# Performance work log

Hardware: AMD Instinct MI355X
Metric: run time of the kernel (lower is better)

Reference implementation:

```python
import jax, jax.numpy as jnp
from jax import lax
import numpy as np


def _gaussian_kernels(k, sigma):
    # spatial Gaussian kernel per sample; sigma: (B,) -> (B, k, k), normalized
    coords = jnp.arange(k) - k // 2
    grid = (coords[None, :] ** 2 + coords[:, None] ** 2).astype(jnp.float32)
    ker = jnp.exp(-grid[None, :, :] / (2.0 * sigma[:, None, None] ** 2))
    return ker / ker.sum(axis=(1, 2), keepdims=True)


def setup_inputs() -> dict:
    key = jax.random.key(0)
    kx, kp = jax.random.split(key)
    x = jax.random.normal(kx, (8, 64, 384, 384), dtype=jnp.float32)
    params = jax.random.normal(kp, (8, 2), dtype=jnp.float32)
    return {"x": x, "params": params}


def reference(x, params):
    B, C, H, W = x.shape
    # torch: params[:,0].long() truncates toward zero, then sigmoid, then int()
    k_int = jnp.trunc(params[:, 0])
    k_sel = jnp.floor(5.0 + 5.0 * jax.nn.sigmoid(k_int)).astype(jnp.int32)  # (B,) in {5..9}
    sigma = 0.5 + 4.5 * jax.nn.sigmoid(params[:, 1])                        # (B,)

    out = jnp.zeros_like(x)
    # small fixed set of possible kernel sizes (structurally distinct convs)
    for k in range(5, 10):
        ker = _gaussian_kernels(k, sigma)  # (B, k, k)
        pad = k // 2

        def conv_one(xi, ki, pad=pad):
            # depthwise conv with the same (k,k) kernel for every channel:
            # treat channels as batch, single-in single-out kernel.
            y = lax.conv_general_dilated(xi[:, None], ki[None, None],
                                         window_strides=(1, 1),
                                         padding=[(pad, pad), (pad, pad)])
            return y[:, 0]

        y = jax.vmap(conv_one)(x, ker)  # (B, C, H', W'); H'=H+1 when k even
        if k % 2 == 0:
            # F.interpolate bilinear align_corners=False == half-pixel, no antialias
            y = jax.image.resize(y, (B, C, H, W), method='bilinear', antialias=False)
        out = jnp.where((k_sel == k)[:, None, None, None], y, out)
    return out
```

## Files before the change

### kernel.cpp

```cpp
#include <hip/hip_runtime.h>
#include <math.h>

#define B_  8
#define C_  64
#define H_  384
#define W_  384

#define TX   64
#define TY   32
#define HALO 4
#define SW   (TX + 2*HALO)
#define SH   (TY + 2*HALO)
#define SWP  76
#define TXP  68

template<int K>
__device__ __forceinline__ void process_tile(
    float (*sIn)[SWP], float (*sTmp)[TXP],
    float* __restrict__ op, int tx0, int ty0, float sigma, int tid)
{
    constexpr int  PAD  = K / 2;
    constexpr bool EVEN = ((K & 1) == 0);

    float g[K];
    {
        const float inv2s2 = 1.0f / (2.0f * sigma * sigma);
        float S = 0.0f;
        #pragma unroll
        for (int i = 0; i < K; ++i) {
            float d = (float)(i - PAD);
            g[i] = expf(-d * d * inv2s2);
            S += g[i];
        }
        const float invS = 1.0f / S;
        #pragma unroll
        for (int i = 0; i < K; ++i) g[i] *= invS;
    }

    for (int li = tid; li < SH * 8; li += 256) {
        const int r  = li >> 3;
        const int g8 = (li & 7) * 8;
        float V[16];
        #pragma unroll
        for (int i = 0; i < 16; ++i) V[i] = sIn[r][g8 + i];
        #pragma unroll
        for (int j = 0; j < 8; ++j) {
            float a0 = 0.0f;
            #pragma unroll
            for (int t = 0; t < K; ++t) a0 += g[t] * V[j + 4 - PAD + t];
            float val = a0;
            if (EVEN) {
                float a1 = 0.0f;
                #pragma unroll
                for (int t = 0; t < K; ++t) a1 += g[t] * V[j + 5 - PAD + t];
                const float fw = ((float)(tx0 + g8 + j) + 0.5f) * (1.0f / (float)W_);
                val = a0 + fw * (a1 - a0);
            }
            sTmp[r][g8 + j] = val;
        }
    }
    __syncthreads();

    for (int li = tid; li < (TY / 4) * 64; li += 256) {
        const int yg = li >> 6;
        const int xx = li & 63;
        float U[12];
        #pragma unroll
        for (int i = 0; i < 12; ++i) U[i] = sTmp[yg * 4 + i][xx];
        #pragma unroll
        for (int j = 0; j < 4; ++j) {
            float a0 = 0.0f;
            #pragma unroll
            for (int t = 0; t < K; ++t) a0 += g[t] * U[j + 4 - PAD + t];
            float val = a0;
            if (EVEN) {
                float a1 = 0.0f;
                #pragma unroll
                for (int t = 0; t < K; ++t) a1 += g[t] * U[j + 5 - PAD + t];
                const float fh = ((float)(ty0 + yg * 4 + j) + 0.5f) * (1.0f / (float)H_);
                val = a0 + fh * (a1 - a0);
            }
            op[(size_t)(ty0 + yg * 4 + j) * W_ + (tx0 + xx)] = val;
        }
    }
}

__global__ __launch_bounds__(256) void gauss_blur_kernel(
    const float* __restrict__ x, const float* __restrict__ params,
    float* __restrict__ out)
{
    const int b    = blockIdx.z;
    const int c    = blockIdx.y;
    const int tile = blockIdx.x;
    const int ntx  = W_ / TX;
    const int tx0  = (tile % ntx) * TX;
    const int ty0  = (tile / ntx) * TY;

    const float p0 = params[2 * b + 0];
    const float p1 = params[2 * b + 1];
    const float k_int = truncf(p0);
    const float s0 = 1.0f / (1.0f + expf(-k_int));
    int k = (int)floorf(5.0f + 5.0f * s0);
    if (k < 5) k = 5;
    if (k > 9) k = 9;
    const float sigma = 0.5f + 4.5f * (1.0f / (1.0f + expf(-p1)));

    __shared__ float sIn[SH][SWP];
    __shared__ float sTmp[SH][TXP];

    const size_t plane = (size_t)(b * C_ + c) * (size_t)(H_ * W_);
    const float* xp = x + plane;
    float*       op = out + plane;
    const int tid = threadIdx.x;

    for (int li = tid; li < SH * (SW / 4); li += 256) {
        const int r  = li / (SW / 4);
        const int c4 = li - r * (SW / 4);
        const int gr = ty0 - HALO + r;
        const int gc = tx0 - HALO + c4 * 4;
        float4 v = make_float4(0.f, 0.f, 0.f, 0.f);
        if (gr >= 0 && gr < H_ && gc >= 0 && gc < W_)
            v = *reinterpret_cast<const float4*>(xp + (size_t)gr * W_ + gc);
        *reinterpret_cast<float4*>(&sIn[r][c4 * 4]) = v;
    }
    __syncthreads();

    switch (k) {
        case 5:  process_tile<5>(sIn, sTmp, op, tx0, ty0, sigma, tid); break;
        case 6:  process_tile<6>(sIn, sTmp, op, tx0, ty0, sigma, tid); break;
        case 7:  process_tile<7>(sIn, sTmp, op, tx0, ty0, sigma, tid); break;
        case 8:  process_tile<8>(sIn, sTmp, op, tx0, ty0, sigma, tid); break;
        default: process_tile<9>(sIn, sTmp, op, tx0, ty0, sigma, tid); break;
    }
}

extern "C" void kernel_launch(void* const* d_in, const int* in_sizes, int n_in,
                              void* d_out, int out_size, void* d_ws, size_t ws_size,
                              hipStream_t stream) {
    const float* x      = (const float*)d_in[0];
    const float* params = (const float*)d_in[1];
    float* out          = (float*)d_out;

    dim3 grid((W_ / TX) * (H_ / TY), C_, B_);
    dim3 block(256, 1, 1);
    gauss_blur_kernel<<<grid, block, 0, stream>>>(x, params, out);
}
```

Measured before the change: 488.7 us.

## Load input directly into registers, enlarge tiles, and remap blocks across XCDs

Drops the shared-memory input staging pass and its barrier. The horizontal pass now reads float4 rows straight from global memory into registers and writes its results to shared memory as float4. Tiles grow to 128x64 with 512-thread blocks, which cuts halo overhead. The grid is flattened and block indices are permuted so that each group of 8 interleaved blocks spans separate contiguous ranges, aiming at XCD/L2 locality. The risk is extra global reads of overlapping halos by neighbouring threads and lower occupancy from the larger blocks.

```diff
diff --git a/kernel.cpp b/kernel.cpp
--- a/kernel.cpp
+++ b/kernel.cpp
@@ -6,18 +6,23 @@
 #define H_  384
 #define W_  384
 
-#define TX   64
-#define TY   32
+#define TX   128
+#define TY   64
 #define HALO 4
-#define SW   (TX + 2*HALO)
 #define SH   (TY + 2*HALO)
-#define SWP  76
-#define TXP  68
+#define TXP  132
+
+#define NTX     (W_ / TX)
+#define NTY     (H_ / TY)
+#define NTILES  (NTX * NTY)
+#define NBLK    (NTILES * C_ * B_)
+
 
 template<int K>
 __device__ __forceinline__ void process_tile(
-    float (*sIn)[SWP], float (*sTmp)[TXP],
-    float* __restrict__ op, int tx0, int ty0, float sigma, int tid)
+    float (*sTmp)[TXP],
+    const float* __restrict__ xp, float* __restrict__ op,
+    int tx0, int ty0, float sigma, int tid)
 {
     constexpr int  PAD  = K / 2;
     constexpr bool EVEN = ((K & 1) == 0);
@@ -37,12 +42,28 @@
         for (int i = 0; i < K; ++i) g[i] *= invS;
     }
 
-    for (int li = tid; li < SH * 8; li += 256) {
-        const int r  = li >> 3;
-        const int g8 = (li & 7) * 8;
+    for (int li = tid; li < SH * (TX / 8); li += 512) {
+        const int r  = li >> 4;
+        const int g8 = (li & 15) * 8;
+        const int gr = ty0 - HALO + r;
+
         float V[16];
-        #pragma unroll
-        for (int i = 0; i < 16; ++i) V[i] = sIn[r][g8 + i];
+        if (gr >= 0 && gr < H_) {
+            const float* rp = xp + (size_t)gr * W_ + (tx0 - HALO + g8);
+            #pragma unroll
+            for (int i = 0; i < 4; ++i) {
+                const int gc = tx0 - HALO + g8 + 4 * i;
+                float4 v = make_float4(0.f, 0.f, 0.f, 0.f);
+                if (gc >= 0 && gc < W_)
+                    v = *reinterpret_cast<const float4*>(rp + 4 * i);
+                V[4*i+0] = v.x; V[4*i+1] = v.y; V[4*i+2] = v.z; V[4*i+3] = v.w;
+            }
+        } else {
+            #pragma unroll
+            for (int i = 0; i < 16; ++i) V[i] = 0.f;
+        }
+
+        float vals[8];
         #pragma unroll
         for (int j = 0; j < 8; ++j) {
             float a0 = 0.0f;
@@ -56,14 +77,16 @@
                 const float fw = ((float)(tx0 + g8 + j) + 0.5f) * (1.0f / (float)W_);
                 val = a0 + fw * (a1 - a0);
             }
-            sTmp[r][g8 + j] = val;
+            vals[j] = val;
         }
+        *reinterpret_cast<float4*>(&sTmp[r][g8])     = make_float4(vals[0], vals[1], vals[2], vals[3]);
+        *reinterpret_cast<float4*>(&sTmp[r][g8 + 4]) = make_float4(vals[4], vals[5], vals[6], vals[7]);
     }
     __syncthreads();
 
-    for (int li = tid; li < (TY / 4) * 64; li += 256) {
-        const int yg = li >> 6;
-        const int xx = li & 63;
+    for (int li = tid; li < (TY / 4) * TX; li += 512) {
+        const int yg = li >> 7;
+        const int xx = li & (TX - 1);
         float U[12];
         #pragma unroll
         for (int i = 0; i < 12; ++i) U[i] = sTmp[yg * 4 + i][xx];
@@ -85,16 +108,20 @@
     }
 }
 
-__global__ __launch_bounds__(256) void gauss_blur_kernel(
+__global__ __launch_bounds__(512) void gauss_blur_kernel(
     const float* __restrict__ x, const float* __restrict__ params,
     float* __restrict__ out)
 {
-    const int b    = blockIdx.z;
-    const int c    = blockIdx.y;
-    const int tile = blockIdx.x;
-    const int ntx  = W_ / TX;
-    const int tx0  = (tile % ntx) * TX;
-    const int ty0  = (tile / ntx) * TY;
+    const int bid  = blockIdx.x;
+    const int gidx = (bid & 7) * (NBLK / 8) + (bid >> 3);
+
+    const int tile = gidx % NTILES;
+    const int bc   = gidx / NTILES;
+    const int c    = bc & (C_ - 1);
+    const int b    = bc >> 6;
+
+    const int tx0 = (tile % NTX) * TX;
+    const int ty0 = (tile / NTX) * TY;
 
     const float p0 = params[2 * b + 0];
     const float p1 = params[2 * b + 1];
@@ -105,7 +132,6 @@
     if (k > 9) k = 9;
     const float sigma = 0.5f + 4.5f * (1.0f / (1.0f + expf(-p1)));
 
-    __shared__ float sIn[SH][SWP];
     __shared__ float sTmp[SH][TXP];
 
     const size_t plane = (size_t)(b * C_ + c) * (size_t)(H_ * W_);
@@ -113,24 +139,12 @@
     float*       op = out + plane;
     const int tid = threadIdx.x;
 
-    for (int li = tid; li < SH * (SW / 4); li += 256) {
-        const int r  = li / (SW / 4);
-        const int c4 = li - r * (SW / 4);
-        const int gr = ty0 - HALO + r;
-        const int gc = tx0 - HALO + c4 * 4;
-        float4 v = make_float4(0.f, 0.f, 0.f, 0.f);
-        if (gr >= 0 && gr < H_ && gc >= 0 && gc < W_)
-            v = *reinterpret_cast<const float4*>(xp + (size_t)gr * W_ + gc);
-        *reinterpret_cast<float4*>(&sIn[r][c4 * 4]) = v;
-    }
-    __syncthreads();
-
     switch (k) {
-        case 5:  process_tile<5>(sIn, sTmp, op, tx0, ty0, sigma, tid); break;
-        case 6:  process_tile<6>(sIn, sTmp, op, tx0, ty0, sigma, tid); break;
-        case 7:  process_tile<7>(sIn, sTmp, op, tx0, ty0, sigma, tid); break;
-        case 8:  process_tile<8>(sIn, sTmp, op, tx0, ty0, sigma, tid); break;
-        default: process_tile<9>(sIn, sTmp, op, tx0, ty0, sigma, tid); break;
+        case 5:  process_tile<5>(sTmp, xp, op, tx0, ty0, sigma, tid); break;
+        case 6:  process_tile<6>(sTmp, xp, op, tx0, ty0, sigma, tid); break;
+        case 7:  process_tile<7>(sTmp, xp, op, tx0, ty0, sigma, tid); break;
+        case 8:  process_tile<8>(sTmp, xp, op, tx0, ty0, sigma, tid); break;
+        default: process_tile<9>(sTmp, xp, op, tx0, ty0, sigma, tid); break;
     }
 }
 
@@ -141,7 +155,7 @@
     const float* params = (const float*)d_in[1];
     float* out          = (float*)d_out;
 
-    dim3 grid((W_ / TX) * (H_ / TY), C_, B_);
-    dim3 block(256, 1, 1);
+    dim3 grid(NBLK, 1, 1);
+    dim3 block(512, 1, 1);
     gauss_blur_kernel<<<grid, block, 0, stream>>>(x, params, out);
 }
```

Result: slower. 506.5 us (+3.6%).
